# Performance work log

Hardware: AMD Instinct MI355X
Metric: run time of the kernel (lower is better)

## Reference

```python
import jax, jax.numpy as jnp
import numpy as np
import math

N_EMBD = 1024
N_HEAD = 16
N_CTX = 2048
SCALE = True
NEG = 1e10


def setup_inputs() -> dict:
    key = jax.random.key(0)
    ks = jax.random.split(key, 4)
    B, S = 2, 2048
    x = jax.random.normal(ks[0], (B, S, N_EMBD), dtype=jnp.float32)
    c_attn_w = jax.random.normal(ks[1], (N_EMBD, 3 * N_EMBD), dtype=jnp.float32) * 0.02
    c_attn_b = jnp.zeros((3 * N_EMBD,), dtype=jnp.float32)
    c_proj_w = jax.random.normal(ks[2], (N_EMBD, N_EMBD), dtype=jnp.float32) * 0.02
    c_proj_b = jnp.zeros((N_EMBD,), dtype=jnp.float32)
    return {"x": x, "c_attn_w": c_attn_w, "c_attn_b": c_attn_b,
            "c_proj_w": c_proj_w, "c_proj_b": c_proj_b}


def reference(x, c_attn_w, c_attn_b, c_proj_w, c_proj_b):
    B, S, D = x.shape
    H = N_HEAD
    hd = D // H
    qkv = x @ c_attn_w + c_attn_b                      # [B,S,3D]
    q, k, v = jnp.split(qkv, 3, axis=-1)
    # split heads -> [B,H,S,hd]
    q = q.reshape(B, S, H, hd).transpose(0, 2, 1, 3)
    k = k.reshape(B, S, H, hd).transpose(0, 2, 1, 3)
    v = v.reshape(B, S, H, hd).transpose(0, 2, 1, 3)
    w = jnp.einsum('bhqd,bhkd->bhqk', q, k)           # [B,H,S,S]
    if SCALE:
        w = w / math.sqrt(hd)
    # multiplicative causal mask trick: w*b - 1e10*(1-b)
    b = jnp.tril(jnp.ones((S, S), dtype=w.dtype))[None, None]
    w = w * b - NEG * (1.0 - b)
    w = jax.nn.softmax(w, axis=-1)
    a = jnp.einsum('bhqk,bhkd->bhqd', w, v)           # [B,H,S,hd]
    a = a.transpose(0, 2, 1, 3).reshape(B, S, D)      # merge heads
    a = a @ c_proj_w + c_proj_b
    present = jnp.stack((k, v))                       # [2,B,H,S,hd]
    return a, present
```

## Files before the change

### kernel.cpp

```cpp
#include <hip/hip_runtime.h>
#include <hip/hip_bf16.h>
#include <cstdint>
#include <cstddef>

#define SEQ 2048
#define DMODEL 1024
#define NHEAD 16
#define HDIM 64
#define MTOT 4096
#define NQKV 3072
#define KDIM 1024

#define OUT_K_BASE  4194304u
#define OUT_V_BASE  8388608u

#define QSCALE 0.18033688011112043f

typedef __attribute__((ext_vector_type(4))) float f32x4;
typedef __attribute__((ext_vector_type(8))) __bf16 bf16x8;
typedef __attribute__((ext_vector_type(8))) short s16x8;
typedef __attribute__((ext_vector_type(4))) short s16x4;
typedef __attribute__((ext_vector_type(2))) int i32x2;

static __device__ __forceinline__ unsigned short f2bf(float f) {
  unsigned int u = __builtin_bit_cast(unsigned int, f);
  u += 0x7FFFu + ((u >> 16) & 1u);
  return (unsigned short)(u >> 16);
}

static __device__ __forceinline__ s16x4 pack4(float4 v) {
  s16x4 r;
  r[0] = (short)f2bf(v.x);
  r[1] = (short)f2bf(v.y);
  r[2] = (short)f2bf(v.z);
  r[3] = (short)f2bf(v.w);
  return r;
}

static __device__ __forceinline__ int cvtpk(float lo, float hi) {
  int r;
  asm("v_cvt_pk_bf16_f32 %0, %1, %2" : "=v"(r) : "v"(lo), "v"(hi));
  return r;
}

static __device__ __forceinline__ f32x4 mfma16(s16x8 a, s16x8 b, f32x4 c) {
  return __builtin_amdgcn_mfma_f32_16x16x32_bf16(
      __builtin_bit_cast(bf16x8, a), __builtin_bit_cast(bf16x8, b), c, 0, 0, 0);
}

static __device__ __forceinline__ void gload16(const void* g, void* l) {
  __builtin_amdgcn_global_load_lds(
      (const __attribute__((address_space(1))) unsigned int*)(uintptr_t)g,
      (__attribute__((address_space(3))) unsigned int*)(uintptr_t)l,
      16, 0, 0);
}

__global__ __launch_bounds__(256) void convert_x(
    const float* __restrict__ X, unsigned short* __restrict__ Xbf)
{
  int i = blockIdx.x * 256 + threadIdx.x;
  float4 v = reinterpret_cast<const float4*>(X)[i];
  reinterpret_cast<s16x4*>(Xbf)[i] = pack4(v);
}

__global__ __launch_bounds__(256) void convert_wt(
    const float* __restrict__ W, unsigned short* __restrict__ Wt, int N)
{
  __shared__ unsigned short t[64][72];
  const int n0 = blockIdx.x * 64, k0 = blockIdx.y * 64;
  const int tid = threadIdx.x;
#pragma unroll
  for (int i = 0; i < 4; ++i) {
    int f = tid + (i << 8);
    int r = f >> 4, c4 = (f & 15) << 2;
    float4 v = *reinterpret_cast<const float4*>(&W[(size_t)(k0 + r) * N + n0 + c4]);
    *reinterpret_cast<s16x4*>(&t[r][c4]) = pack4(v);
  }
  __syncthreads();
#pragma unroll
  for (int i = 0; i < 2; ++i) {
    int g = tid + (i << 8);
    int n = g >> 3, k8 = (g & 7) << 3;
    s16x8 o;
#pragma unroll
    for (int jj = 0; jj < 8; ++jj) o[jj] = (short)t[k8 + jj][n];
    *reinterpret_cast<s16x8*>(&Wt[(size_t)(n0 + n) * KDIM + k0 + k8]) = o;
  }
}

#define GEMM_MAIN_LOOP(Aptr, Btptr)                                           \
  const int tid = threadIdx.x;                                                \
  const int lane = tid & 63;                                                  \
  const int wv = tid >> 6;                                                    \
  const int wr = wv >> 1, wc = wv & 1;                                        \
  const int m0 = blockIdx.x * 128;                                            \
  const int n0 = blockIdx.y * 128;                                            \
  const int lr = lane & 15;                                                   \
  const int gq = lane >> 4;                                                   \
  const f32x4 fzero = {0.f, 0.f, 0.f, 0.f};                                   \
  f32x4 acc[4][4];                                                            \
  _Pragma("unroll") for (int i = 0; i < 4; ++i)                               \
      _Pragma("unroll") for (int j = 0; j < 4; ++j) acc[i][j] = fzero;        \
  {                                                                           \
    const int ar0 = tid >> 2;                                                 \
    const int ar1 = ar0 + 64;                                                 \
    const int ac0 = (((tid & 3) ^ ((ar0 >> 1) & 3)) << 3);                    \
    const int ub0 = wv << 9;                                                  \
    const int ub1 = 2048 + (wv << 9);                                         \
    auto stage = [&](int nb, int kk) {                                        \
      gload16(&(Aptr)[(size_t)(m0 + ar0) * KDIM + kk + ac0],                  \
              &lds_a[nb][0][0] + ub0);                                        \
      gload16(&(Aptr)[(size_t)(m0 + ar1) * KDIM + kk + ac0],                  \
              &lds_a[nb][0][0] + ub1);                                        \
      gload16(&(Btptr)[(size_t)(n0 + ar0) * KDIM + kk + ac0],                 \
              &lds_b[nb][0][0] + ub0);                                        \
      gload16(&(Btptr)[(size_t)(n0 + ar1) * KDIM + kk + ac0],                 \
              &lds_b[nb][0][0] + ub1);                                        \
    };                                                                        \
    stage(0, 0);                                                              \
    const int fsw = ((lr >> 1) & 3);                                          \
    for (int t = 0; t < 32; ++t) {                                            \
      __syncthreads();              \
      if (t < 31) stage((t + 1) & 1, (t + 1) << 5);                           \
      const int bufg = t & 1;                                                 \
      s16x8 af[4], bfv[4];                                                    \
      _Pragma("unroll") for (int mi = 0; mi < 4; ++mi)                        \
          af[mi] = *reinterpret_cast<const s16x8*>(                           \
              &lds_a[bufg][wr * 64 + mi * 16 + lr][(gq ^ fsw) << 3]);         \
      _Pragma("unroll") for (int ni = 0; ni < 4; ++ni)                        \
          bfv[ni] = *reinterpret_cast<const s16x8*>(                          \
              &lds_b[bufg][wc * 64 + ni * 16 + lr][(gq ^ fsw) << 3]);         \
      _Pragma("unroll") for (int ni = 0; ni < 4; ++ni)                        \
          _Pragma("unroll") for (int mi = 0; mi < 4; ++mi)                    \
              acc[mi][ni] = mfma16(af[mi], bfv[ni], acc[mi][ni]);             \
    }                                                                         \
  }

__global__ __launch_bounds__(256) void qkv_gemm(
    const unsigned short* __restrict__ Xbf,
    const unsigned short* __restrict__ Wt,
    const float* __restrict__ Bias,
    float* out,
    unsigned short* __restrict__ Qbf)
{
  __shared__ __align__(16) unsigned short lds_a[2][128][32];
  __shared__ __align__(16) unsigned short lds_b[2][128][32];

  unsigned short* Kbf = (unsigned short*)out;
  unsigned short* Vt  = Kbf + 4194304;

  GEMM_MAIN_LOOP(Xbf, Wt)

  const int seg = n0 >> 10;

  if (seg == 0) {
#pragma unroll
    for (int ni = 0; ni < 4; ++ni) {
      int c = n0 + wc * 64 + ni * 16 + lr;
      float bias = Bias[c];
      int h = (c & 1023) >> 6, d = c & 63;
#pragma unroll
      for (int mi = 0; mi < 4; ++mi)
#pragma unroll
        for (int j = 0; j < 4; ++j) {
          int m = m0 + wr * 64 + mi * 16 + gq * 4 + j;
          int b = m >> 11, s = m & 2047;
          Qbf[(size_t)((b * NHEAD + h) * SEQ + s) * HDIM + d] =
              f2bf((acc[mi][ni][j] + bias) * QSCALE);
        }
    }
  } else if (seg == 1) {
#pragma unroll
    for (int ni = 0; ni < 4; ++ni) {
      int c = n0 + wc * 64 + ni * 16 + lr;
      float bias = Bias[c];
      int h = (c & 1023) >> 6, d = c & 63;
#pragma unroll
      for (int mi = 0; mi < 4; ++mi)
#pragma unroll
        for (int j = 0; j < 4; ++j) {
          int m = m0 + wr * 64 + mi * 16 + gq * 4 + j;
          int b = m >> 11, s = m & 2047;
          float val = acc[mi][ni][j] + bias;
          size_t idx = (size_t)((b * NHEAD + h) * SEQ + s) * HDIM + d;
          out[OUT_K_BASE + idx] = val;
          Kbf[idx] = f2bf(val);
        }
    }
  } else {
    __syncthreads();
    unsigned short* T = (wv < 2) ? (&lds_a[0][0][0] + (wv << 12))
                                 : (&lds_b[0][0][0] + ((wv - 2) << 12));
    const int b = m0 >> 11;
    const int s0 = (m0 & 2047) + wr * 64;
    const int h = (n0 >> 6) - 32 + wc;
#pragma unroll
    for (int ni = 0; ni < 4; ++ni) {
      int c = n0 + wc * 64 + ni * 16 + lr;
      float bias = Bias[c];
      int d_loc = ni * 16 + lr;
      int dsw = d_loc & 7;
#pragma unroll
      for (int mi = 0; mi < 4; ++mi)
#pragma unroll
        for (int j = 0; j < 4; ++j) {
          int s_loc = mi * 16 + gq * 4 + j;
          float val = acc[mi][ni][j] + bias;
          out[OUT_V_BASE +
              (size_t)((b * NHEAD + h) * SEQ + s0 + s_loc) * HDIM + d_loc] = val;
          T[d_loc * 64 + ((((s_loc >> 3) ^ dsw)) << 3) + (s_loc & 7)] = f2bf(val);
        }
    }
#pragma unroll
    for (int it = 0; it < 8; ++it) {
      int dl = (lane >> 3) + (it << 3);
      int cl = lane & 7;
      s16x8 vv = *reinterpret_cast<const s16x8*>(
          &T[dl * 64 + ((cl ^ (dl & 7)) << 3)]);
      size_t vi = (((size_t)(b * NHEAD + h) * HDIM + dl) << 11) + s0 + (cl << 3);
      *reinterpret_cast<s16x8*>(&Vt[vi]) = vv;
    }
  }
}

__global__ __launch_bounds__(256) void proj_gemm(
    const unsigned short* __restrict__ Abf,
    const unsigned short* __restrict__ Wpt,
    const float* __restrict__ Bias,
    float* __restrict__ out)
{
  __shared__ __align__(16) unsigned short lds_a[2][128][32];
  __shared__ __align__(16) unsigned short lds_b[2][128][32];

  GEMM_MAIN_LOOP(Abf, Wpt)

#pragma unroll
  for (int ni = 0; ni < 4; ++ni) {
    int c = n0 + wc * 64 + ni * 16 + lr;
    float bias = Bias[c];
#pragma unroll
    for (int mi = 0; mi < 4; ++mi) {
#pragma unroll
      for (int j = 0; j < 4; ++j) {
        int m = m0 + wr * 64 + mi * 16 + gq * 4 + j;
        out[(size_t)m * DMODEL + c] = acc[mi][ni][j] + bias;
      }
    }
  }
}

__global__ __launch_bounds__(256, 4) void attn_fwd(
    const unsigned short* __restrict__ Qbf,
    const unsigned short* __restrict__ Kbf,
    const unsigned short* __restrict__ Vtg,
    unsigned short* __restrict__ Abf)
{
  __shared__ __align__(16) unsigned short K_lds[2][64][64];
  __shared__ __align__(16) unsigned short V_lds[2][64][64];
  __shared__ __align__(16) unsigned short P_lds[4][16][64];

  const int tid = threadIdx.x;
  const int lane = tid & 63;
  const int wv = tid >> 6;
  const int bid = blockIdx.x;
  const int qt = 31 - (bid >> 5);
  const int bh = bid & 31;

  const int lr = lane & 15;
  const int gq = lane >> 4;

  const unsigned short* Kg = Kbf + (size_t)bh * (SEQ * HDIM);
  const unsigned short* Vg = Vtg + (size_t)bh * (SEQ * HDIM);
  const unsigned short* Qg = Qbf + (size_t)bh * (SEQ * HDIM)
                                 + (size_t)(qt * 64 + wv * 16) * HDIM;

  s16x8 qf0 = *reinterpret_cast<const s16x8*>(&Qg[lr * 64 + (gq << 3)]);
  s16x8 qf1 = *reinterpret_cast<const s16x8*>(&Qg[lr * 64 + 32 + (gq << 3)]);

  const f32x4 fzero = {0.f, 0.f, 0.f, 0.f};
  f32x4 O[4];
  float mrow = -1e30f, lrow = 0.f;
#pragma unroll
  for (int no = 0; no < 4; ++no) O[no] = fzero;

#define STAGE(kv0, nb)                                                        \
  {                                                                           \
    _Pragma("unroll")                                                         \
    for (int i = 0; i < 2; ++i) {                                             \
      int L = tid + (i << 8);                                                 \
      int r = L >> 3, c = L & 7;                                              \
      int cc = (c ^ (r & 7)) << 3;                                            \
      int ubase = ((i << 8) + (wv << 6)) << 3;                                \
      gload16(&Kg[(((kv0) + r) << 6) + cc], &K_lds[nb][0][0] + ubase);        \
      gload16(&Vg[((size_t)r << 11) + (kv0) + cc], &V_lds[nb][0][0] + ubase); \
    }                                                                         \
  }

  STAGE(0, 0);

  for (int t = 0; t <= qt; ++t) {
    __syncthreads();
    if (t < qt) STAGE((t + 1) * 64, (t + 1) & 1);
    const int buf = t & 1;

    f32x4 sc[4];
#pragma unroll
    for (int ni = 0; ni < 4; ++ni) {
      int kr = ni * 16 + lr;
      int sw = kr & 7;
      s16x8 kb0 = *reinterpret_cast<const s16x8*>(&K_lds[buf][kr][(gq ^ sw) << 3]);
      s16x8 kb1 = *reinterpret_cast<const s16x8*>(&K_lds[buf][kr][((gq + 4) ^ sw) << 3]);
      f32x4 tacc = mfma16(kb0, qf0, fzero);
      sc[ni] = mfma16(kb1, qf1, tacc);
    }

    if (t == qt) {
      int qloc = wv * 16 + lr;
#pragma unroll
      for (int ni = 0; ni < 4; ++ni)
#pragma unroll
        for (int r = 0; r < 4; ++r)
          if (ni * 16 + gq * 4 + r > qloc) sc[ni][r] = -1e30f;
    }

    float tmax = fmaxf(fmaxf(fmaxf(sc[0][0], sc[0][1]), fmaxf(sc[0][2], sc[0][3])),
                       fmaxf(fmaxf(sc[1][0], sc[1][1]), fmaxf(sc[1][2], sc[1][3])));
    tmax = fmaxf(tmax,
                 fmaxf(fmaxf(fmaxf(sc[2][0], sc[2][1]), fmaxf(sc[2][2], sc[2][3])),
                       fmaxf(fmaxf(sc[3][0], sc[3][1]), fmaxf(sc[3][2], sc[3][3]))));
    tmax = fmaxf(tmax, __shfl_xor(tmax, 16));
    tmax = fmaxf(tmax, __shfl_xor(tmax, 32));
    float newm = fmaxf(mrow, tmax);
    float fs = __builtin_amdgcn_exp2f(mrow - newm);
    mrow = newm;
    float rs = 0.f;
#pragma unroll
    for (int ni = 0; ni < 4; ++ni) {
#pragma unroll
      for (int r = 0; r < 4; ++r) {
        float p = __builtin_amdgcn_exp2f(sc[ni][r] - newm);
        sc[ni][r] = p;
        rs += p;
      }
    }
    rs += __shfl_xor(rs, 16);
    rs += __shfl_xor(rs, 32);
    lrow = lrow * fs + rs;
#pragma unroll
    for (int no = 0; no < 4; ++no) O[no] *= fs;

    {
      unsigned short* Prow = &P_lds[wv][lr][0];
      const int swl = lr & 7;
#pragma unroll
      for (int ni = 0; ni < 4; ++ni) {
        i32x2 d2;
        d2[0] = cvtpk(sc[ni][0], sc[ni][1]);
        d2[1] = cvtpk(sc[ni][2], sc[ni][3]);
        int off = ((((2 * ni) + (gq >> 1)) ^ swl) << 3) + ((gq & 1) << 2);
        *reinterpret_cast<i32x2*>(&Prow[off]) = d2;
      }
      s16x8 pB0 = *reinterpret_cast<const s16x8*>(&Prow[(gq ^ swl) << 3]);
      s16x8 pB1 = *reinterpret_cast<const s16x8*>(&Prow[((gq + 4) ^ swl) << 3]);

#pragma unroll
      for (int no = 0; no < 4; ++no) {
        int dr = no * 16 + lr;
        int sw = dr & 7;
        s16x8 vb0 = *reinterpret_cast<const s16x8*>(&V_lds[buf][dr][(gq ^ sw) << 3]);
        s16x8 vb1 = *reinterpret_cast<const s16x8*>(&V_lds[buf][dr][((gq + 4) ^ sw) << 3]);
        O[no] = mfma16(vb0, pB0, O[no]);
        O[no] = mfma16(vb1, pB1, O[no]);
      }
    }
  }

  const int b = bh >> 4, h = bh & 15;
  float inv = 1.0f / lrow;
  int srow = qt * 64 + wv * 16 + lr;
  size_t base = (size_t)(b * SEQ + srow) * DMODEL + h * 64 + (gq << 2);
#pragma unroll
  for (int no = 0; no < 4; ++no) {
    s16x4 ov;
#pragma unroll
    for (int r = 0; r < 4; ++r) ov[r] = (short)f2bf(O[no][r] * inv);
    *reinterpret_cast<s16x4*>(&Abf[base + no * 16]) = ov;
  }
#undef STAGE
}

extern "C" void kernel_launch(void* const* d_in, const int* in_sizes, int n_in,
                              void* d_out, int out_size, void* d_ws, size_t ws_size,
                              hipStream_t stream) {
  const float* x        = (const float*)d_in[0];
  const float* c_attn_w = (const float*)d_in[1];
  const float* c_attn_b = (const float*)d_in[2];
  const float* c_proj_w = (const float*)d_in[3];
  const float* c_proj_b = (const float*)d_in[4];
  float* out = (float*)d_out;

  unsigned short* Qbf = (unsigned short*)d_ws;
  unsigned short* Xbf = Qbf + 4194304;
  unsigned short* Abf = Xbf;
  unsigned short* Wt  = Qbf + 8388608;
  unsigned short* Wpt = Wt;
  unsigned short* Kbf = (unsigned short*)out;
  unsigned short* Vt  = Kbf + 4194304;

  convert_x<<<dim3(4096), 256, 0, stream>>>(x, Xbf);
  convert_wt<<<dim3(48, 16), 256, 0, stream>>>(c_attn_w, Wt, NQKV);
  qkv_gemm<<<dim3(32, 24), 256, 0, stream>>>(Xbf, Wt, c_attn_b, out, Qbf);
  convert_wt<<<dim3(16, 16), 256, 0, stream>>>(c_proj_w, Wpt, DMODEL);
  attn_fwd<<<dim3(1024), 256, 0, stream>>>(Qbf, Kbf, Vt, Abf);
  proj_gemm<<<dim3(32, 8), 256, 0, stream>>>(Abf, Wpt, c_proj_b, out);
}
```

Baseline: 120.3 us.

## Enlarge QKV GEMM tile to 256x256 and deepen proj GEMM K-step to 64

The QKV GEMM moves from 128x128 tiles with 256 threads to 256x256 tiles with 512 threads and 8x4 MFMA accumulators per wave. This raises data reuse per LDS load and cuts global traffic. The V-transpose epilogue is split into two halves so it fits the existing LDS scratch. The projection GEMM keeps 128x128 tiles but stages 64-wide K slices with an 8-way XOR swizzle, halving the number of barriers. The trade-offs are fewer blocks for QKV (192, below the CU count), higher register pressure, and more LDS per block.

```diff
diff --git a/kernel.cpp b/kernel.cpp
--- a/kernel.cpp
+++ b/kernel.cpp
@@ -88,68 +88,73 @@
   }
 }
 
-#define GEMM_MAIN_LOOP(Aptr, Btptr)                                           \
-  const int tid = threadIdx.x;                                                \
-  const int lane = tid & 63;                                                  \
-  const int wv = tid >> 6;                                                    \
-  const int wr = wv >> 1, wc = wv & 1;                                        \
-  const int m0 = blockIdx.x * 128;                                            \
-  const int n0 = blockIdx.y * 128;                                            \
-  const int lr = lane & 15;                                                   \
-  const int gq = lane >> 4;                                                   \
-  const f32x4 fzero = {0.f, 0.f, 0.f, 0.f};                                   \
-  f32x4 acc[4][4];                                                            \
-  _Pragma("unroll") for (int i = 0; i < 4; ++i)                               \
-      _Pragma("unroll") for (int j = 0; j < 4; ++j) acc[i][j] = fzero;        \
-  {                                                                           \
-    const int ar0 = tid >> 2;                                                 \
-    const int ar1 = ar0 + 64;                                                 \
-    const int ac0 = (((tid & 3) ^ ((ar0 >> 1) & 3)) << 3);                    \
-    const int ub0 = wv << 9;                                                  \
-    const int ub1 = 2048 + (wv << 9);                                         \
-    auto stage = [&](int nb, int kk) {                                        \
-      gload16(&(Aptr)[(size_t)(m0 + ar0) * KDIM + kk + ac0],                  \
-              &lds_a[nb][0][0] + ub0);                                        \
-      gload16(&(Aptr)[(size_t)(m0 + ar1) * KDIM + kk + ac0],                  \
-              &lds_a[nb][0][0] + ub1);                                        \
-      gload16(&(Btptr)[(size_t)(n0 + ar0) * KDIM + kk + ac0],                 \
-              &lds_b[nb][0][0] + ub0);                                        \
-      gload16(&(Btptr)[(size_t)(n0 + ar1) * KDIM + kk + ac0],                 \
-              &lds_b[nb][0][0] + ub1);                                        \
-    };                                                                        \
-    stage(0, 0);                                                              \
-    const int fsw = ((lr >> 1) & 3);                                          \
-    for (int t = 0; t < 32; ++t) {                                            \
-      __syncthreads();              \
-      if (t < 31) stage((t + 1) & 1, (t + 1) << 5);                           \
-      const int bufg = t & 1;                                                 \
-      s16x8 af[4], bfv[4];                                                    \
-      _Pragma("unroll") for (int mi = 0; mi < 4; ++mi)                        \
-          af[mi] = *reinterpret_cast<const s16x8*>(                           \
-              &lds_a[bufg][wr * 64 + mi * 16 + lr][(gq ^ fsw) << 3]);         \
-      _Pragma("unroll") for (int ni = 0; ni < 4; ++ni)                        \
-          bfv[ni] = *reinterpret_cast<const s16x8*>(                          \
-              &lds_b[bufg][wc * 64 + ni * 16 + lr][(gq ^ fsw) << 3]);         \
-      _Pragma("unroll") for (int ni = 0; ni < 4; ++ni)                        \
-          _Pragma("unroll") for (int mi = 0; mi < 4; ++mi)                    \
-              acc[mi][ni] = mfma16(af[mi], bfv[ni], acc[mi][ni]);             \
-    }                                                                         \
-  }
-
-__global__ __launch_bounds__(256) void qkv_gemm(
+__global__ __launch_bounds__(512, 2) void qkv_gemm(
     const unsigned short* __restrict__ Xbf,
     const unsigned short* __restrict__ Wt,
     const float* __restrict__ Bias,
     float* out,
     unsigned short* __restrict__ Qbf)
 {
-  __shared__ __align__(16) unsigned short lds_a[2][128][32];
-  __shared__ __align__(16) unsigned short lds_b[2][128][32];
+  __shared__ __align__(16) unsigned short lds_a[2][256][32];
+  __shared__ __align__(16) unsigned short lds_b[2][256][32];
 
   unsigned short* Kbf = (unsigned short*)out;
   unsigned short* Vt  = Kbf + 4194304;
 
-  GEMM_MAIN_LOOP(Xbf, Wt)
+  const int tid = threadIdx.x;
+  const int lane = tid & 63;
+  const int wv = tid >> 6;
+  const int wr = wv >> 2;
+  const int wc = wv & 3;
+  const int m0 = blockIdx.x * 256;
+  const int n0 = blockIdx.y * 256;
+  const int lr = lane & 15;
+  const int gq = lane >> 4;
+
+  const f32x4 fzero = {0.f, 0.f, 0.f, 0.f};
+  f32x4 acc[8][4];
+#pragma unroll
+  for (int i = 0; i < 8; ++i)
+#pragma unroll
+    for (int j = 0; j < 4; ++j) acc[i][j] = fzero;
+
+  {
+    const int r0 = tid >> 2;
+    const int r1 = r0 + 128;
+    const int c0 = tid & 3;
+    const int sc0 = ((c0 ^ ((r0 >> 1) & 3)) << 3);
+    const int sc1 = ((c0 ^ ((r1 >> 1) & 3)) << 3);
+    const int ub0 = (wv << 6) << 3;
+    const int ub1 = ((1 << 9) + (wv << 6)) << 3;
+    auto stage = [&](int nb, int kk) {
+      gload16(&Xbf[(size_t)(m0 + r0) * KDIM + kk + sc0], &lds_a[nb][0][0] + ub0);
+      gload16(&Xbf[(size_t)(m0 + r1) * KDIM + kk + sc1], &lds_a[nb][0][0] + ub1);
+      gload16(&Wt[(size_t)(n0 + r0) * KDIM + kk + sc0], &lds_b[nb][0][0] + ub0);
+      gload16(&Wt[(size_t)(n0 + r1) * KDIM + kk + sc1], &lds_b[nb][0][0] + ub1);
+    };
+    stage(0, 0);
+    for (int t = 0; t < 32; ++t) {
+      __syncthreads();
+      if (t < 31) stage((t + 1) & 1, (t + 1) << 5);
+      const int bufg = t & 1;
+      s16x8 bfv[4];
+#pragma unroll
+      for (int ni = 0; ni < 4; ++ni) {
+        int row = wc * 64 + ni * 16 + lr;
+        bfv[ni] = *reinterpret_cast<const s16x8*>(
+            &lds_b[bufg][row][(gq ^ ((row >> 1) & 3)) << 3]);
+      }
+#pragma unroll
+      for (int mi = 0; mi < 8; ++mi) {
+        int row = wr * 128 + mi * 16 + lr;
+        s16x8 af = *reinterpret_cast<const s16x8*>(
+            &lds_a[bufg][row][(gq ^ ((row >> 1) & 3)) << 3]);
+#pragma unroll
+        for (int ni = 0; ni < 4; ++ni)
+          acc[mi][ni] = mfma16(af, bfv[ni], acc[mi][ni]);
+      }
+    }
+  }
 
   const int seg = n0 >> 10;
 
@@ -160,10 +165,10 @@
       float bias = Bias[c];
       int h = (c & 1023) >> 6, d = c & 63;
 #pragma unroll
-      for (int mi = 0; mi < 4; ++mi)
+      for (int mi = 0; mi < 8; ++mi)
 #pragma unroll
         for (int j = 0; j < 4; ++j) {
-          int m = m0 + wr * 64 + mi * 16 + gq * 4 + j;
+          int m = m0 + wr * 128 + mi * 16 + gq * 4 + j;
           int b = m >> 11, s = m & 2047;
           Qbf[(size_t)((b * NHEAD + h) * SEQ + s) * HDIM + d] =
               f2bf((acc[mi][ni][j] + bias) * QSCALE);
@@ -176,10 +181,10 @@
       float bias = Bias[c];
       int h = (c & 1023) >> 6, d = c & 63;
 #pragma unroll
-      for (int mi = 0; mi < 4; ++mi)
+      for (int mi = 0; mi < 8; ++mi)
 #pragma unroll
         for (int j = 0; j < 4; ++j) {
-          int m = m0 + wr * 64 + mi * 16 + gq * 4 + j;
+          int m = m0 + wr * 128 + mi * 16 + gq * 4 + j;
           int b = m >> 11, s = m & 2047;
           float val = acc[mi][ni][j] + bias;
           size_t idx = (size_t)((b * NHEAD + h) * SEQ + s) * HDIM + d;
@@ -189,36 +194,43 @@
     }
   } else {
     __syncthreads();
-    unsigned short* T = (wv < 2) ? (&lds_a[0][0][0] + (wv << 12))
-                                 : (&lds_b[0][0][0] + ((wv - 2) << 12));
+    unsigned short* T = (wv < 4) ? (&lds_a[0][0][0] + (wv << 12))
+                                 : (&lds_b[0][0][0] + ((wv - 4) << 12));
     const int b = m0 >> 11;
-    const int s0 = (m0 & 2047) + wr * 64;
+    const int s0 = (m0 & 2047) + wr * 128;
     const int h = (n0 >> 6) - 32 + wc;
 #pragma unroll
-    for (int ni = 0; ni < 4; ++ni) {
-      int c = n0 + wc * 64 + ni * 16 + lr;
-      float bias = Bias[c];
-      int d_loc = ni * 16 + lr;
-      int dsw = d_loc & 7;
-#pragma unroll
-      for (int mi = 0; mi < 4; ++mi)
-#pragma unroll
-        for (int j = 0; j < 4; ++j) {
-          int s_loc = mi * 16 + gq * 4 + j;
-          float val = acc[mi][ni][j] + bias;
-          out[OUT_V_BASE +
-              (size_t)((b * NHEAD + h) * SEQ + s0 + s_loc) * HDIM + d_loc] = val;
-          T[d_loc * 64 + ((((s_loc >> 3) ^ dsw)) << 3) + (s_loc & 7)] = f2bf(val);
+    for (int h2 = 0; h2 < 2; ++h2) {
+#pragma unroll
+      for (int ni = 0; ni < 4; ++ni) {
+        int c = n0 + wc * 64 + ni * 16 + lr;
+        float bias = Bias[c];
+        int d_loc = ni * 16 + lr;
+        int dsw = d_loc & 7;
+#pragma unroll
+        for (int mh = 0; mh < 4; ++mh) {
+          int mi = h2 * 4 + mh;
+#pragma unroll
+          for (int j = 0; j < 4; ++j) {
+            int s_loc = mi * 16 + gq * 4 + j;
+            int ss = s_loc - (h2 << 6);
+            float val = acc[mi][ni][j] + bias;
+            out[OUT_V_BASE +
+                (size_t)((b * NHEAD + h) * SEQ + s0 + s_loc) * HDIM + d_loc] = val;
+            T[d_loc * 64 + (((ss >> 3) ^ dsw) << 3) + (ss & 7)] = f2bf(val);
+          }
         }
-    }
-#pragma unroll
-    for (int it = 0; it < 8; ++it) {
-      int dl = (lane >> 3) + (it << 3);
-      int cl = lane & 7;
-      s16x8 vv = *reinterpret_cast<const s16x8*>(
-          &T[dl * 64 + ((cl ^ (dl & 7)) << 3)]);
-      size_t vi = (((size_t)(b * NHEAD + h) * HDIM + dl) << 11) + s0 + (cl << 3);
-      *reinterpret_cast<s16x8*>(&Vt[vi]) = vv;
+      }
+#pragma unroll
+      for (int it = 0; it < 8; ++it) {
+        int dl = (lane >> 3) + (it << 3);
+        int cl = lane & 7;
+        s16x8 vv = *reinterpret_cast<const s16x8*>(
+            &T[dl * 64 + ((cl ^ (dl & 7)) << 3)]);
+        size_t vi = (((size_t)(b * NHEAD + h) * HDIM + dl) << 11) +
+                    s0 + (h2 << 6) + (cl << 3);
+        *reinterpret_cast<s16x8*>(&Vt[vi]) = vv;
+      }
     }
   }
 }
@@ -229,10 +241,64 @@
     const float* __restrict__ Bias,
     float* __restrict__ out)
 {
-  __shared__ __align__(16) unsigned short lds_a[2][128][32];
-  __shared__ __align__(16) unsigned short lds_b[2][128][32];
-
-  GEMM_MAIN_LOOP(Abf, Wpt)
+  __shared__ __align__(16) unsigned short lds_a[2][128][64];
+  __shared__ __align__(16) unsigned short lds_b[2][128][64];
+
+  const int tid = threadIdx.x;
+  const int lane = tid & 63;
+  const int wv = tid >> 6;
+  const int wr = wv >> 1, wc = wv & 1;
+  const int m0 = blockIdx.x * 128;
+  const int n0 = blockIdx.y * 128;
+  const int lr = lane & 15;
+  const int gq = lane >> 4;
+
+  const f32x4 fzero = {0.f, 0.f, 0.f, 0.f};
+  f32x4 acc[4][4];
+#pragma unroll
+  for (int i = 0; i < 4; ++i)
+#pragma unroll
+    for (int j = 0; j < 4; ++j) acc[i][j] = fzero;
+
+  {
+    const int r0 = tid >> 3;
+    const int c0 = tid & 7;
+    auto stage = [&](int nb, int kk) {
+#pragma unroll
+      for (int i = 0; i < 4; ++i) {
+        int r = r0 + (i << 5);
+        int sc = ((c0 ^ (r & 7)) << 3);
+        int ub = (((i << 8) + (wv << 6)) << 3);
+        gload16(&Abf[(size_t)(m0 + r) * KDIM + kk + sc], &lds_a[nb][0][0] + ub);
+        gload16(&Wpt[(size_t)(n0 + r) * KDIM + kk + sc], &lds_b[nb][0][0] + ub);
+      }
+    };
+    stage(0, 0);
+    for (int t = 0; t < 16; ++t) {
+      __syncthreads();
+      if (t < 15) stage((t + 1) & 1, (t + 1) << 6);
+      const int bufg = t & 1;
+#pragma unroll
+      for (int kf = 0; kf < 2; ++kf) {
+        s16x8 bfv[4];
+#pragma unroll
+        for (int ni = 0; ni < 4; ++ni) {
+          int row = wc * 64 + ni * 16 + lr;
+          bfv[ni] = *reinterpret_cast<const s16x8*>(
+              &lds_b[bufg][row][((kf * 4 + gq) ^ (row & 7)) << 3]);
+        }
+#pragma unroll
+        for (int mi = 0; mi < 4; ++mi) {
+          int row = wr * 64 + mi * 16 + lr;
+          s16x8 af = *reinterpret_cast<const s16x8*>(
+              &lds_a[bufg][row][((kf * 4 + gq) ^ (row & 7)) << 3]);
+#pragma unroll
+          for (int ni = 0; ni < 4; ++ni)
+            acc[mi][ni] = mfma16(af, bfv[ni], acc[mi][ni]);
+        }
+      }
+    }
+  }
 
 #pragma unroll
   for (int ni = 0; ni < 4; ++ni) {
@@ -409,7 +475,7 @@
 
   convert_x<<<dim3(4096), 256, 0, stream>>>(x, Xbf);
   convert_wt<<<dim3(48, 16), 256, 0, stream>>>(c_attn_w, Wt, NQKV);
-  qkv_gemm<<<dim3(32, 24), 256, 0, stream>>>(Xbf, Wt, c_attn_b, out, Qbf);
+  qkv_gemm<<<dim3(16, 12), 512, 0, stream>>>(Xbf, Wt, c_attn_b, out, Qbf);
   convert_wt<<<dim3(16, 16), 256, 0, stream>>>(c_proj_w, Wpt, DMODEL);
   attn_fwd<<<dim3(1024), 256, 0, stream>>>(Qbf, Kbf, Vt, Abf);
   proj_gemm<<<dim3(32, 8), 256, 0, stream>>>(Abf, Wpt, c_proj_b, out);
```

New measurement: 111.3 us. -7.5%, faster.
